# Optimization experiments

Measured on AMD Instinct MI355X. Metric: run time of the kernel, lower is better.

The kernel has to match this reference:

```python
import jax, jax.numpy as jnp
import numpy as np

BETA = 2.0 / 3.0
GAMMA = -0.1
ZETA = 1.1

T, B, I, H = 512, 64, 512, 768


def setup_inputs() -> dict:
    key = jax.random.key(0)
    ks = jax.random.split(key, 6)
    stdv = 1.0 / np.sqrt(H)
    x = jax.random.normal(ks[0], (T, B, I), dtype=jnp.float32)
    W = jax.random.uniform(ks[1], (4 * H, I), dtype=jnp.float32, minval=-stdv, maxval=stdv)
    U = jax.random.uniform(ks[2], (4 * H, H), dtype=jnp.float32, minval=-stdv, maxval=stdv)
    b = jax.random.uniform(ks[3], (4 * H,), dtype=jnp.float32, minval=-stdv, maxval=stdv)
    # log_alpha_s init: normal(mean=1, std=0.1)
    log_alpha = 1.0 + 0.1 * jax.random.normal(ks[4], (H,), dtype=jnp.float32)
    # one uniform draw per timestep for the stochastic L0 gate (torch.rand_like)
    u = jax.random.uniform(ks[5], (T, H), dtype=jnp.float32, minval=1e-6, maxval=1.0 - 1e-6)
    return {"x": x, "W": W, "U": U, "b": b, "log_alpha": log_alpha, "u": u}


def reference(x, W, U, b, log_alpha, u):
    # x: [T,B,I] seq-first. Training-path masked LSTM with stochastic gate.
    Bsz = x.shape[1]
    Hs = log_alpha.shape[0]
    # Precompute input projection: x @ W.T -> [T,B,4H].
    # Note W_hat = W * srep[:,None], so x @ W_hat.T == (x @ W.T) * srep,
    # and the * srep is applied inside the step (fused with b term).
    x_proj = jnp.einsum('tbi,gi->tbg', x, W)

    def step(carry, inp):
        hx, cx = carry
        xp, u_t = inp  # xp: [B,4H], u_t: [H]
        # hard-concrete / L0 smooth gate
        tau_hat = jax.nn.sigmoid((jnp.log(u_t) - jnp.log1p(-u_t) + log_alpha) / BETA)
        s = jnp.clip(tau_hat * (ZETA - GAMMA) + GAMMA, 0.0, 1.0)  # [H]
        srep = jnp.tile(s, 4)  # [4H]
        # U_hat = U * outer(srep, s) => hx @ U_hat.T == ((hx*s) @ U.T) * srep
        gates = (xp + (hx * s) @ U.T + b) * srep  # [B,4H]
        ig, fg, cg, og = jnp.split(gates, 4, axis=-1)
        ig = jax.nn.sigmoid(ig) * s
        fg = jax.nn.sigmoid(fg) * s
        cg = jnp.tanh(cg) * s
        og = jax.nn.sigmoid(og) * s
        cy = fg * cx + ig * cg
        hy = og * jnp.tanh(cy)
        return (hy, cy), hy

    h0 = jnp.zeros((Bsz, Hs), dtype=x.dtype)
    c0 = jnp.zeros((Bsz, Hs), dtype=x.dtype)
    _, ys = jax.lax.scan(step, (h0, c0), (x_proj, u))
    return ys  # [T,B,H]
```

## Files before the change

kernel.cpp:

```cpp
#include <hip/hip_runtime.h>
#include <cstdint>
#include <cstddef>

#define T_STEPS 512
#define BATCH   64
#define IN_DIM  512
#define HID     768
#define G4H     3072
#define NROWS   32768
#define HPLANE  49152
#define DBUFB   98304

typedef __attribute__((ext_vector_type(8))) _Float16 f16x8;
typedef __attribute__((ext_vector_type(4))) float f32x4;

__device__ __forceinline__ float sigmoidf_(float z){ return 1.0f/(1.0f+expf(-z)); }
__device__ __forceinline__ unsigned short f16_bits(float v){
    return __builtin_bit_cast(unsigned short, (_Float16)v);
}
__device__ __forceinline__ float h16_to_f(unsigned u){
    return (float)__builtin_bit_cast(_Float16, (unsigned short)(u & 0xffffu));
}

__global__ void cvt_f16_kernel(const float* __restrict__ in, _Float16* __restrict__ out, int n){
    int i = blockIdx.x*256 + threadIdx.x;
    if (i < n) out[i] = (_Float16)in[i];
}

__global__ void gate_s_kernel(const float* __restrict__ u, const float* __restrict__ la,
                              float* __restrict__ s_all, int n){
    int i = blockIdx.x*256 + threadIdx.x;
    if (i < n){
        int h = i % HID;
        float uu = u[i];
        float lg = (logf(uu) - log1pf(-uu) + la[h]) * 1.5f;
        s_all[i] = fminf(fmaxf(1.2f*sigmoidf_(lg) - 0.1f, 0.f), 1.f);
    }
}

__global__ __launch_bounds__(256, 4) void xproj_gemm_t(
    const _Float16* __restrict__ A, const _Float16* __restrict__ B,
    unsigned short* __restrict__ CT)
{
    const int wave = threadIdx.x >> 6;
    const int lane = threadIdx.x & 63;
    const int tile = blockIdx.x*4 + wave;
    const int mt = tile & 511;
    const int nt = tile >> 9;
    const long m0 = (long)mt*64, n0 = (long)nt*64;
    const int lr = lane & 15, lq = lane >> 4;

    f32x4 acc[4][4];
    #pragma unroll
    for (int i=0;i<4;i++)
        #pragma unroll
        for (int j=0;j<4;j++) acc[i][j] = (f32x4){0.f,0.f,0.f,0.f};

    const _Float16* Ap = A + (m0 + lr)*512 + lq*8;
    const _Float16* Bp = B + (n0 + lr)*512 + lq*8;

    for (int k0 = 0; k0 < 512; k0 += 32){
        f16x8 a[4], b[4];
        #pragma unroll
        for (int i=0;i<4;i++) a[i] = *(const f16x8*)(Ap + (long)i*16*512 + k0);
        #pragma unroll
        for (int j=0;j<4;j++) b[j] = *(const f16x8*)(Bp + (long)j*16*512 + k0);
        #pragma unroll
        for (int i=0;i<4;i++)
            #pragma unroll
            for (int j=0;j<4;j++)
                acc[i][j] = __builtin_amdgcn_mfma_f32_16x16x32_f16(a[i], b[j], acc[i][j], 0,0,0);
    }

    #pragma unroll
    for (int i=0;i<4;i++)
        #pragma unroll
        for (int j=0;j<4;j++){
            long col = n0 + 16*j + lr;
            long rb  = m0 + 16*i + lq*4;
            unsigned long long pk =
                  (unsigned long long)f16_bits(acc[i][j][0])
                | ((unsigned long long)f16_bits(acc[i][j][1]) << 16)
                | ((unsigned long long)f16_bits(acc[i][j][2]) << 32)
                | ((unsigned long long)f16_bits(acc[i][j][3]) << 48);
            *(unsigned long long*)(CT + col*NROWS + rb) = pk;
        }
}

__global__ __launch_bounds__(512, 1) void lstm_scan11(
    const float* __restrict__ U,
    const float* __restrict__ bias,
    const float* __restrict__ s_all,
    const _Float16* __restrict__ xpT,
    float* __restrict__ out,
    char* __restrict__ hbuf,
    unsigned int* __restrict__ bar)
{
    __shared__ float sRed[2*32*33 + 4];
    __shared__ char  sPad[77824];

    const int tid = threadIdx.x;
    const int bx  = blockIdx.x;
    const int bg  = bx & 1;
    const int cb  = bx >> 1;
    const int hc0 = 6*cb;
    const int row0 = 32*bg;

    const int w    = tid >> 6;
    const int lane = tid & 63;
    const int ks2  = w & 1;
    const int mt   = (w >> 1) & 1;
    const int nt   = (w >> 2) & 1;
    const int lr   = lane & 15;
    const int kq   = lane >> 4;
    const int mrow = mt*16 + lr;

    if (tid == 0) ((volatile char*)sPad)[0] = 0;

    f16x8 Bf[12];
    {
        const int c = nt*16 + lr;
        #pragma unroll
        for (int i=0;i<12;i++){
            const int kb = ks2*12 + i;
            f16x8 v = {0,0,0,0,0,0,0,0};
            if (c < 24){
                const int g = c/6, jj = c - 6*g;
                const float* up = U + (size_t)(g*HID + hc0 + jj)*HID + kb*32 + kq*8;
                #pragma unroll
                for (int e=0;e<8;e++) v[e] = (_Float16)up[e];
            }
            Bf[i] = v;
        }
    }

    const bool own = tid < 192;
    const int orow = tid & 31;
    const int oj   = tid >> 5;
    const int ohc  = hc0 + (oj < 6 ? oj : 0);
    float c_state = 0.f;
    float b0=0.f,b1=0.f,b2=0.f,b3=0.f;
    float s_cur=0.f, s_nextF=0.f;
    float xvf0=0.f,xvf1=0.f,xvf2=0.f,xvf3=0.f;
    unsigned xr0=0,xr1=0,xr2=0,xr3=0,snr=0;
    const char *xp0=nullptr,*xp1=nullptr,*xp2=nullptr,*xp3=nullptr,*spp=nullptr;
    if (own){
        b0 = bias[ohc]; b1 = bias[HID+ohc]; b2 = bias[2*HID+ohc]; b3 = bias[3*HID+ohc];
        const size_t trow0 = (size_t)row0 + orow;
        xp0 = (const char*)(xpT + (size_t)(0*HID+ohc)*NROWS + trow0);
        xp1 = (const char*)(xpT + (size_t)(1*HID+ohc)*NROWS + trow0);
        xp2 = (const char*)(xpT + (size_t)(2*HID+ohc)*NROWS + trow0);
        xp3 = (const char*)(xpT + (size_t)(3*HID+ohc)*NROWS + trow0);
        spp = (const char*)(s_all + ohc);
        xvf0 = (float)*(const _Float16*)xp0;
        xvf1 = (float)*(const _Float16*)xp1;
        xvf2 = (float)*(const _Float16*)xp2;
        xvf3 = (float)*(const _Float16*)xp3;
        s_cur   = s_all[ohc];
        s_nextF = s_all[HID + ohc];
    }
    __syncthreads();

    for (int t = 0; t < T_STEPS; ++t){
        const char* gsrc = hbuf + (size_t)(t&1)*DBUFB + (size_t)bg*HPLANE;

        f32x4 ar[12];
        #pragma unroll
        for (int i=0;i<12;i++){
            const int kb = ks2*12 + i;
            const char* ap = gsrc + (size_t)(((kb*4 + kq)*32 + mrow)*16);
            asm volatile("global_load_dwordx4 %0, %1, off sc0 sc1" : "=v"(ar[i]) : "v"(ap));
        }
        asm volatile("s_waitcnt vmcnt(0)"
            : "+v"(ar[0]),"+v"(ar[1]),"+v"(ar[2]),"+v"(ar[3]),"+v"(ar[4]),"+v"(ar[5]),
              "+v"(ar[6]),"+v"(ar[7]),"+v"(ar[8]),"+v"(ar[9]),"+v"(ar[10]),"+v"(ar[11])
            :: "memory");
        __builtin_amdgcn_sched_barrier(0);

        f32x4 acA = {0.f,0.f,0.f,0.f};
        f32x4 acB = {0.f,0.f,0.f,0.f};
        #pragma unroll
        for (int i=0;i<6;i++){
            acA = __builtin_amdgcn_mfma_f32_16x16x32_f16(
                      __builtin_bit_cast(f16x8, ar[i]),   Bf[i],   acA, 0,0,0);
            acB = __builtin_amdgcn_mfma_f32_16x16x32_f16(
                      __builtin_bit_cast(f16x8, ar[6+i]), Bf[6+i], acB, 0,0,0);
        }
        f32x4 acc = acA + acB;

        {
            float* rp = sRed + (size_t)(ks2*32 + nt*16 + lr)*33 + mt*16 + kq*4;
            *(f32x4*)rp = acc;
        }
        __syncthreads();

        if (own){
            if (t){
                s_cur   = s_nextF;
                s_nextF = __builtin_bit_cast(float, snr);
                xvf0 = h16_to_f(xr0); xvf1 = h16_to_f(xr1);
                xvf2 = h16_to_f(xr2); xvf3 = h16_to_f(xr3);
            }
            const int c0_ = 0*6 + oj, c1_ = 1*6 + oj, c2_ = 2*6 + oj, c3_ = 3*6 + oj;
            float p0 = xvf0 + b0 + sRed[(size_t)c0_*33 + orow] + sRed[(size_t)(32+c0_)*33 + orow];
            float p1 = xvf1 + b1 + sRed[(size_t)c1_*33 + orow] + sRed[(size_t)(32+c1_)*33 + orow];
            float p2 = xvf2 + b2 + sRed[(size_t)c2_*33 + orow] + sRed[(size_t)(32+c2_)*33 + orow];
            float p3 = xvf3 + b3 + sRed[(size_t)c3_*33 + orow] + sRed[(size_t)(32+c3_)*33 + orow];
            const float s = s_cur;
            p0 *= s; p1 *= s; p2 *= s; p3 *= s;
            float ig = sigmoidf_(p0)*s;
            float fg = sigmoidf_(p1)*s;
            float cg = tanhf(p2)*s;
            float og = sigmoidf_(p3)*s;
            c_state = fg*c_state + ig*cg;
            float h = og*tanhf(c_state);
            out[((size_t)t*BATCH + row0 + orow)*HID + ohc] = h;
            if (t+1 < T_STEPS){
                float hs = h * s_nextF;
                unsigned int hv = f16_bits(hs);
                char* dst = hbuf + (size_t)((t+1)&1)*DBUFB + (size_t)bg*HPLANE
                          + 2*(size_t)(((ohc>>3)*32 + orow)*8 + (ohc&7));
                asm volatile("global_store_short %0, %1, off sc0 sc1"
                             :: "v"(dst), "v"(hv) : "memory");
            }
        }

        if (t+1 < T_STEPS){
            asm volatile("s_waitcnt vmcnt(0)" ::: "memory");
            __syncthreads();
            if (own){
                const size_t off = (size_t)(t+1)*BATCH*2;
                const int ts = (t+2 < T_STEPS) ? (t+2) : (T_STEPS-1);
                const char* sp = spp + (size_t)ts*HID*4;
                asm volatile("global_load_ushort %0, %1, off" : "=v"(xr0) : "v"(xp0 + off));
                asm volatile("global_load_ushort %0, %1, off" : "=v"(xr1) : "v"(xp1 + off));
                asm volatile("global_load_ushort %0, %1, off" : "=v"(xr2) : "v"(xp2 + off));
                asm volatile("global_load_ushort %0, %1, off" : "=v"(xr3) : "v"(xp3 + off));
                asm volatile("global_load_dword %0, %1, off"  : "=v"(snr) : "v"(sp));
            }
            if (tid == 0){
                const unsigned cell = (unsigned)((bg*4 + (cb&3))*32);
                __hip_atomic_fetch_add(bar + cell, 1u, __ATOMIC_RELAXED, __HIP_MEMORY_SCOPE_AGENT);
                const unsigned tgt = (unsigned)(t+1)*128u;
                for (;;){
                    unsigned ssum = 0;
                    #pragma unroll
                    for (int c2=0;c2<4;c2++)
                        ssum += __hip_atomic_load(bar + (bg*4+c2)*32, __ATOMIC_RELAXED, __HIP_MEMORY_SCOPE_AGENT);
                    if (ssum >= tgt) break;
                    __builtin_amdgcn_s_sleep(1);
                }
            }
            __syncthreads();
        }
    }
}

extern "C" void kernel_launch(void* const* d_in, const int* in_sizes, int n_in,
                              void* d_out, int out_size, void* d_ws, size_t ws_size,
                              hipStream_t stream){
    const float* x  = (const float*)d_in[0];
    const float* W  = (const float*)d_in[1];
    const float* U  = (const float*)d_in[2];
    const float* b  = (const float*)d_in[3];
    const float* la = (const float*)d_in[4];
    const float* u  = (const float*)d_in[5];
    float* out = (float*)d_out;

    char* ws = (char*)d_ws;
    char*           hbuf  = ws;
    unsigned int*   bar   = (unsigned int*)(ws + 196608);
    _Float16*       xf16  = (_Float16*)(ws + 200704);
    float*          s_all = (float*)(ws + 200704);
    _Float16*       wf16  = (_Float16*)(ws + 200704 + 33554432);
    unsigned short* xpT   = (unsigned short*)(ws + 36900864);

    hipMemsetAsync(d_ws, 0, 200704, stream);

    cvt_f16_kernel<<<65536, 256, 0, stream>>>(x, xf16, NROWS*IN_DIM);
    cvt_f16_kernel<<<6144,  256, 0, stream>>>(W, wf16, G4H*IN_DIM);
    xproj_gemm_t<<<6144, 256, 0, stream>>>(xf16, wf16, xpT);
    gate_s_kernel<<<1536, 256, 0, stream>>>(u, la, s_all, T_STEPS*HID);
    lstm_scan11<<<256, 512, 0, stream>>>(U, b, s_all, (const _Float16*)xpT, out, hbuf, bar);
}
```

Baseline: 2.518 ms.

## Use fast gate math, spread grid barrier counters, and swizzle GEMM tiles

The LSTM scan switches sigmoid and tanh to hardware exp2/rcp approximations, which shortens the serial per-step latency at some cost in accuracy. The grid barrier now uses 16 counters per batch group instead of 4, and 16 threads each poll one counter rather than a single thread summing all of them. This is meant to cut atomic contention and barrier latency on every one of the 512 steps. The x-projection GEMM also remaps tiles into panels of 8 M-tiles so concurrently running blocks share operand data in L2.

Measured after the change: 2.608 ms. +3.6%, slower.

```diff
diff --git a/kernel.cpp b/kernel.cpp
--- a/kernel.cpp
+++ b/kernel.cpp
@@ -15,6 +15,12 @@
 typedef __attribute__((ext_vector_type(4))) float f32x4;
 
 __device__ __forceinline__ float sigmoidf_(float z){ return 1.0f/(1.0f+expf(-z)); }
+__device__ __forceinline__ float sigmoid_fast(float z){
+    return __builtin_amdgcn_rcpf(1.0f + __builtin_amdgcn_exp2f(-1.44269504f * z));
+}
+__device__ __forceinline__ float tanh_fast(float x){
+    return 1.0f - 2.0f*__builtin_amdgcn_rcpf(1.0f + __builtin_amdgcn_exp2f(2.88539008f * x));
+}
 __device__ __forceinline__ unsigned short f16_bits(float v){
     return __builtin_bit_cast(unsigned short, (_Float16)v);
 }
@@ -44,9 +50,14 @@
 {
     const int wave = threadIdx.x >> 6;
     const int lane = threadIdx.x & 63;
-    const int tile = blockIdx.x*4 + wave;
-    const int mt = tile & 511;
-    const int nt = tile >> 9;
+    const int bx   = blockIdx.x;
+    const int x8   = bx & 7;
+    const int i8   = bx >> 3;
+    const int panel = x8 + 8*(i8/12);
+    const int sub   = i8 % 12;
+    const int tile  = panel*48 + sub*4 + wave;
+    const int mt = tile / 48;
+    const int nt = tile % 48;
     const long m0 = (long)mt*64, n0 = (long)nt*64;
     const int lr = lane & 15, lq = lane >> 4;
 
@@ -87,7 +98,7 @@
         }
 }
 
-__global__ __launch_bounds__(512, 1) void lstm_scan11(
+__global__ __launch_bounds__(512, 1) void lstm_scan12(
     const float* __restrict__ U,
     const float* __restrict__ bias,
     const float* __restrict__ s_all,
@@ -208,12 +219,12 @@
             float p3 = xvf3 + b3 + sRed[(size_t)c3_*33 + orow] + sRed[(size_t)(32+c3_)*33 + orow];
             const float s = s_cur;
             p0 *= s; p1 *= s; p2 *= s; p3 *= s;
-            float ig = sigmoidf_(p0)*s;
-            float fg = sigmoidf_(p1)*s;
-            float cg = tanhf(p2)*s;
-            float og = sigmoidf_(p3)*s;
+            float ig = sigmoid_fast(p0)*s;
+            float fg = sigmoid_fast(p1)*s;
+            float cg = tanh_fast(p2)*s;
+            float og = sigmoid_fast(p3)*s;
             c_state = fg*c_state + ig*cg;
-            float h = og*tanhf(c_state);
+            float h = og*tanh_fast(c_state);
             out[((size_t)t*BATCH + row0 + orow)*HID + ohc] = h;
             if (t+1 < T_STEPS){
                 float hs = h * s_nextF;
@@ -239,17 +250,14 @@
                 asm volatile("global_load_dword %0, %1, off"  : "=v"(snr) : "v"(sp));
             }
             if (tid == 0){
-                const unsigned cell = (unsigned)((bg*4 + (cb&3))*32);
+                const unsigned cell = (unsigned)((bg*16 + (cb&15))*32);
                 __hip_atomic_fetch_add(bar + cell, 1u, __ATOMIC_RELAXED, __HIP_MEMORY_SCOPE_AGENT);
-                const unsigned tgt = (unsigned)(t+1)*128u;
-                for (;;){
-                    unsigned ssum = 0;
-                    #pragma unroll
-                    for (int c2=0;c2<4;c2++)
-                        ssum += __hip_atomic_load(bar + (bg*4+c2)*32, __ATOMIC_RELAXED, __HIP_MEMORY_SCOPE_AGENT);
-                    if (ssum >= tgt) break;
+            }
+            if (tid < 16){
+                const unsigned tgt = (unsigned)(t+1)*8u;
+                const unsigned int* cp = bar + (bg*16 + tid)*32;
+                while (__hip_atomic_load(cp, __ATOMIC_RELAXED, __HIP_MEMORY_SCOPE_AGENT) < tgt)
                     __builtin_amdgcn_s_sleep(1);
-                }
             }
             __syncthreads();
         }
@@ -281,5 +289,5 @@
     cvt_f16_kernel<<<6144,  256, 0, stream>>>(W, wf16, G4H*IN_DIM);
     xproj_gemm_t<<<6144, 256, 0, stream>>>(xf16, wf16, xpT);
     gate_s_kernel<<<1536, 256, 0, stream>>>(u, la, s_all, T_STEPS*HID);
-    lstm_scan11<<<256, 512, 0, stream>>>(U, b, s_all, (const _Float16*)xpT, out, hbuf, bar);
-}
+    lstm_scan12<<<256, 512, 0, stream>>>(U, b, s_all, (const _Float16*)xpT, out, hbuf, bar);
+}
```
